# Kernel optimization log

Hardware: AMD Instinct MI355X
Metric: run time of the kernel (lower is better)

Reference implementation:

```python
import jax, jax.numpy as jnp
import numpy as np

B, C, H, W = 8, 96, 56, 56
N = H * W
K = 9
COUT = 2 * C  # 192


def setup_inputs() -> dict:
    key = jax.random.key(0)
    ks = jax.random.split(key, 12)
    s = 0.05
    inp = {
        "x": jax.random.normal(ks[0], (B, C, H, W), jnp.float32),
        "kmap_w": jax.random.normal(ks[1], (C, 500), jnp.float32) * s,
        "kmap_b": jnp.zeros((500,), jnp.float32),
        "kfc_w": jax.random.normal(ks[2], (500, 64), jnp.float32) * s,
        "kfc_b": jnp.zeros((64,), jnp.float32),
        "kmu_w": jax.random.normal(ks[3], (64, 32), jnp.float32) * s,
        "kmu_b": jnp.zeros((32,), jnp.float32),
        "kdec_w": jax.random.normal(ks[4], (32, K), jnp.float32) * s,
        "kdec_b": jnp.zeros((K,), jnp.float32),
        "ec1_w": jax.random.normal(ks[5], (2 * C, C), jnp.float32) * s,
        "ec1_b": jnp.zeros((C,), jnp.float32),
        "ec2_w": jax.random.normal(ks[6], (2 * C, C), jnp.float32) * s,
        "ec2_b": jnp.zeros((C,), jnp.float32),
        "fc_w": jax.random.normal(ks[7], (C, COUT), jnp.float32) * s,
        "fc_b": jnp.zeros((COUT,), jnp.float32),
        "io_w": jax.random.normal(ks[8], (C, COUT), jnp.float32) * s,
        "io_b": jnp.zeros((COUT,), jnp.float32),
        "up_w": jax.random.normal(ks[9], (2 * COUT, COUT), jnp.float32) * s,
        "up_b": jnp.zeros((COUT,), jnp.float32),
    }
    return inp


def reference(x, kmap_w, kmap_b, kfc_w, kfc_b, kmu_w, kmu_b, kdec_w, kdec_b,
              ec1_w, ec1_b, ec2_w, ec2_b, fc_w, fc_b, io_w, io_b, up_w, up_b):
    b, c, h, w = x.shape
    n = h * w
    xf = x.reshape(b, c, n).transpose(0, 2, 1)  # [B, N, C]

    # ---- dense kNN graph (dilation=1, deterministic) ----
    sq = jnp.sum(xf * xf, axis=-1)  # [B, N]
    dist = sq[:, :, None] - 2.0 * jnp.einsum('bnc,bmc->bnm', xf, xf) + sq[:, None, :]
    _, nn_idx = jax.lax.top_k(-dist, K)  # [B, N, K] local neighbor indices

    nodes = xf.reshape(b * n, c)  # flat node features

    # ---- VAE-like K predictor -> per-node kept-degree (non-differentiable) ----
    hK = nodes @ kmap_w + kmap_b
    hK = jax.nn.relu(hK @ kfc_w + kfc_b)
    mu = hK @ kmu_w + kmu_b
    logits = mu @ kdec_w + kdec_b  # [B*N, K]
    k_int = jnp.argmax(logits, axis=1)  # in [0, K-1]

    # edge mask: keep first k_int[i] of node i's K edges
    edge_mask = (jnp.arange(K)[None, :] < k_int[:, None]).reshape(-1)  # [B*N*K]
    emask = edge_mask.astype(nodes.dtype)[:, None]

    # flatten edges with per-batch node offsets (local -> global indices)
    offs = (jnp.arange(b) * n)[:, None, None]
    src = (nn_idx + offs).reshape(-1)              # x_j
    dst = jnp.repeat(jnp.arange(b * n), K)         # x_i (center)

    def edge_conv(feat, wgt, bias):
        xi = feat[dst]
        xj = feat[src]
        msg = jnp.concatenate([xi, xj - xi], axis=-1) @ wgt + bias
        msg = msg * emask  # pruned edges contribute 0 to 'add' aggregation
        return jax.ops.segment_sum(msg, dst, num_segments=b * n)

    h1 = jax.nn.relu(edge_conv(nodes, ec1_w, ec1_b))
    h2 = edge_conv(h1, ec2_w, ec2_b)
    agg = h2 @ fc_w + fc_b                 # EdgeAgg output [B*N, COUT]

    xio = nodes @ io_w + io_b              # inOutFC
    upd = jax.nn.relu(jnp.concatenate([xio, agg], axis=-1) @ up_w + up_b)

    out = upd.reshape(b, n, 2 * c).transpose(0, 2, 1).reshape(b, 2 * c, h, w)
    return out
```

## Files before the change

kernel.cpp:

```cpp
#include <hip/hip_runtime.h>

#define NODES 25088
#define NB 8
#define NPB 3136
#define C 96
#define KNN 9
#define COUT 192
#define MSPLIT 4
#define T12 12
#define NCAND (MSPLIT * T12)

typedef float f32x4 __attribute__((ext_vector_type(4)));
typedef float f32x16 __attribute__((ext_vector_type(16)));
typedef short s16x8 __attribute__((ext_vector_type(8)));

__device__ __forceinline__ unsigned short f2bf(float x) {
  unsigned u = __float_as_uint(x);
  return (unsigned short)((u + 0x7fffu + ((u >> 16) & 1u)) >> 16);
}
__device__ __forceinline__ float bf2f(unsigned short h) {
  return __uint_as_float(((unsigned)h) << 16);
}

__global__ void transpose_kernel(const float* __restrict__ x, float* __restrict__ xf) {
  __shared__ float t[32][33];
  int b = blockIdx.z, ct = blockIdx.y, nt = blockIdx.x;
  int tx = threadIdx.x, ty = threadIdx.y;
  int n0 = nt * 32, c0 = ct * 32;
  const float* xb = x + (size_t)b * C * NPB;
#pragma unroll
  for (int i = 0; i < 4; i++) {
    int c = c0 + ty + i * 8;
    t[ty + i * 8][tx] = xb[(size_t)c * NPB + n0 + tx];
  }
  __syncthreads();
  float* xfb = xf + (size_t)b * NPB * C;
#pragma unroll
  for (int i = 0; i < 4; i++) {
    int n = n0 + ty + i * 8;
    xfb[(size_t)n * C + c0 + tx] = t[tx][ty + i * 8];
  }
}

__global__ void sqsplit_kernel(const float* __restrict__ xf, float* __restrict__ sq,
                               unsigned short* __restrict__ xh,
                               unsigned short* __restrict__ xl) {
  int node = blockIdx.x * 256 + threadIdx.x;
  const float4* r = (const float4*)(xf + (size_t)node * C);
  ushort4* hp = (ushort4*)(xh + (size_t)node * C);
  ushort4* lp = (ushort4*)(xl + (size_t)node * C);
  float s = 0.f;
#pragma unroll
  for (int i = 0; i < 24; i++) {
    float4 v = r[i];
    s += v.x * v.x + v.y * v.y + v.z * v.z + v.w * v.w;
    ushort4 h, l;
    h.x = f2bf(v.x); l.x = f2bf(v.x - bf2f(h.x));
    h.y = f2bf(v.y); l.y = f2bf(v.y - bf2f(h.y));
    h.z = f2bf(v.z); l.z = f2bf(v.z - bf2f(h.z));
    h.w = f2bf(v.w); l.w = f2bf(v.w - bf2f(h.w));
    hp[i] = h;
    lp[i] = l;
  }
  sq[node] = s;
}

__global__ void fold_all_kernel(
    const float* __restrict__ kmap_w, const float* __restrict__ kmap_b,
    const float* __restrict__ kfc_w, const float* __restrict__ kfc_b,
    const float* __restrict__ kmu_w, const float* __restrict__ kmu_b,
    const float* __restrict__ kdec_w, const float* __restrict__ kdec_b,
    const float* __restrict__ ec1_w, const float* __restrict__ ec2_w,
    const float* __restrict__ io_w, const float* __restrict__ io_b,
    const float* __restrict__ fc_w, const float* __restrict__ fc_b,
    const float* __restrict__ up_w, const float* __restrict__ up_b,
    float* __restrict__ WkP, float* __restrict__ bkP, float* __restrict__ WdP,
    float* __restrict__ bdP, float* __restrict__ bPf,
    unsigned short* __restrict__ B1h, unsigned short* __restrict__ B1l,
    unsigned short* __restrict__ B2h, unsigned short* __restrict__ B2l,
    unsigned short* __restrict__ BFh, unsigned short* __restrict__ BFl) {
  __shared__ float sh[4][64];
  int bid = blockIdx.x, tid = threadIdx.x;
  int tx = tid & 63, ty = tid >> 6;
  if (bid < 96) {
    int m = bid;
    float acc = 0.f;
    for (int k = ty; k < 500; k += 4) acc += kmap_w[m * 500 + k] * kfc_w[k * 64 + tx];
    sh[ty][tx] = acc;
    __syncthreads();
    if (ty == 0) WkP[m * 64 + tx] = sh[0][tx] + sh[1][tx] + sh[2][tx] + sh[3][tx];
  } else if (bid == 96) {
    float acc = 0.f;
    for (int k = ty; k < 500; k += 4) acc += kmap_b[k] * kfc_w[k * 64 + tx];
    sh[ty][tx] = acc;
    __syncthreads();
    if (ty == 0) bkP[tx] = sh[0][tx] + sh[1][tx] + sh[2][tx] + sh[3][tx] + kfc_b[tx];
  } else if (bid < 161) {
    int m = bid - 97;
    float acc = 0.f;
    if (tx < 9) {
      for (int k = ty; k < 32; k += 4) acc += kmu_w[m * 32 + k] * kdec_w[k * 9 + tx];
    }
    sh[ty][tx] = acc;
    __syncthreads();
    if (ty == 0 && tx < 9) WdP[m * 9 + tx] = sh[0][tx] + sh[1][tx] + sh[2][tx] + sh[3][tx];
  } else if (bid == 161) {
    float acc = 0.f;
    if (tx < 9) {
      for (int k = ty; k < 32; k += 4) acc += kmu_b[k] * kdec_w[k * 9 + tx];
    }
    sh[ty][tx] = acc;
    __syncthreads();
    if (ty == 0 && tx < 9) bdP[tx] = sh[0][tx] + sh[1][tx] + sh[2][tx] + sh[3][tx] + kdec_b[tx];
  } else if (bid < 234) {
    int t = (bid - 162) * 256 + tid;
    int n = t / 192, k = t % 192;
    float v = ec1_w[(size_t)k * 96 + n];
    if (k < 96) v -= ec1_w[(size_t)(k + 96) * 96 + n];
    unsigned short h = f2bf(v);
    B1h[t] = h;
    B1l[t] = f2bf(v - bf2f(h));
  } else if (bid < 306) {
    int t = (bid - 234) * 256 + tid;
    int n = t / 192, k = t % 192;
    float v = ec2_w[(size_t)k * 96 + n];
    if (k < 96) v -= ec2_w[(size_t)(k + 96) * 96 + n];
    unsigned short h = f2bf(v);
    B2h[t] = h;
    B2l[t] = f2bf(v - bf2f(h));
  } else if (bid < 594) {
    int r = bid - 306;
    int m = r / 3, n = (r % 3) * 64 + tx;
    float acc = 0.f;
    for (int k = ty; k < 192; k += 4) acc += io_w[m * 192 + k] * up_w[(size_t)k * 192 + n];
    sh[ty][tx] = acc;
    __syncthreads();
    if (ty == 0) {
      float v = sh[0][tx] + sh[1][tx] + sh[2][tx] + sh[3][tx];
      unsigned short h = f2bf(v);
      BFh[(size_t)n * 192 + m] = h;
      BFl[(size_t)n * 192 + m] = f2bf(v - bf2f(h));
    }
  } else if (bid < 882) {
    int r = bid - 594;
    int m = r / 3, n = (r % 3) * 64 + tx;
    float acc = 0.f;
    for (int k = ty; k < 192; k += 4)
      acc += fc_w[m * 192 + k] * up_w[(size_t)(192 + k) * 192 + n];
    sh[ty][tx] = acc;
    __syncthreads();
    if (ty == 0) {
      float v = sh[0][tx] + sh[1][tx] + sh[2][tx] + sh[3][tx];
      unsigned short h = f2bf(v);
      BFh[(size_t)n * 192 + 96 + m] = h;
      BFl[(size_t)n * 192 + 96 + m] = f2bf(v - bf2f(h));
    }
  } else {
    if (tid < 192) {
      float acc = up_b[tid];
      for (int k = 0; k < 192; k++) {
        acc += io_b[k] * up_w[k * 192 + tid];
        acc += fc_b[k] * up_w[(192 + k) * 192 + tid];
      }
      bPf[tid] = acc;
    }
  }
}

__global__ __launch_bounds__(256) void gemmhead_kernel(
    const float* __restrict__ A0, const float* __restrict__ B,
    const float* __restrict__ bias, const float* __restrict__ WdP,
    const float* __restrict__ bdP, int* __restrict__ kint,
    float* __restrict__ rs) {
  __shared__ float As[16][68];
  __shared__ float Bs[16][68];
  __shared__ float hs[64][68];
  __shared__ float wd[576];
  __shared__ float bd[9];
  int tid = threadIdx.x;
  int tx = tid & 15, ty = tid >> 4;
  int row0 = blockIdx.x * 64;
  for (int f = tid; f < 576; f += 256) wd[f] = WdP[f];
  if (tid < 9) bd[tid] = bdP[tid];
  float acc[4][4] = {};
  int ai = tid >> 2;
  int ak = (tid & 3) * 4;
  int bk = tid >> 4;
  int bj = (tid & 15) * 4;

  for (int k0 = 0; k0 < 96; k0 += 16) {
    {
      int r = row0 + ai;
      float4 v = *(const float4*)(A0 + (size_t)r * 96 + k0 + ak);
      As[ak + 0][ai] = v.x;
      As[ak + 1][ai] = v.y;
      As[ak + 2][ai] = v.z;
      As[ak + 3][ai] = v.w;
    }
    {
      int kg = k0 + bk;
      float4 v = *(const float4*)(B + (size_t)kg * 64 + bj);
      *(float4*)&Bs[bk][bj] = v;
    }
    __syncthreads();
#pragma unroll
    for (int kk = 0; kk < 16; kk++) {
      float4 av = *(const float4*)&As[kk][ty * 4];
      float4 bv = *(const float4*)&Bs[kk][tx * 4];
      acc[0][0] += av.x * bv.x; acc[0][1] += av.x * bv.y; acc[0][2] += av.x * bv.z; acc[0][3] += av.x * bv.w;
      acc[1][0] += av.y * bv.x; acc[1][1] += av.y * bv.y; acc[1][2] += av.y * bv.z; acc[1][3] += av.y * bv.w;
      acc[2][0] += av.z * bv.x; acc[2][1] += av.z * bv.y; acc[2][2] += av.z * bv.z; acc[2][3] += av.z * bv.w;
      acc[3][0] += av.w * bv.x; acc[3][1] += av.w * bv.y; acc[3][2] += av.w * bv.z; acc[3][3] += av.w * bv.w;
    }
    __syncthreads();
  }
#pragma unroll
  for (int ii = 0; ii < 4; ii++) {
#pragma unroll
    for (int jj = 0; jj < 4; jj++) {
      int j = tx * 4 + jj;
      hs[ty * 4 + ii][j] = fmaxf(acc[ii][jj] + bias[j], 0.f);
    }
  }
  __syncthreads();
  if (tid < 64) {
    int node = row0 + tid;
    const float4* hp = (const float4*)hs[tid];
    float4 h[16];
#pragma unroll
    for (int i = 0; i < 16; i++) h[i] = hp[i];
    float best = -3.4e38f;
    int bi = 0;
#pragma unroll
    for (int n = 0; n < 9; n++) {
      float a = bd[n];
#pragma unroll
      for (int k = 0; k < 16; k++) {
        float4 hv = h[k];
        a += hv.x * wd[(4 * k + 0) * 9 + n] + hv.y * wd[(4 * k + 1) * 9 + n] +
             hv.z * wd[(4 * k + 2) * 9 + n] + hv.w * wd[(4 * k + 3) * 9 + n];
      }
      if (a > best) { best = a; bi = n; }
    }
    kint[node] = bi;
    rs[node] = (float)bi;
  }
}

__device__ __forceinline__ void ce(float& a, float& b) {
  float lo = fminf(a, b);
  b = fmaxf(a, b);
  a = lo;
}

__device__ __forceinline__ void sort16(float* s) {
  ce(s[0], s[1]); ce(s[2], s[3]); ce(s[0], s[2]); ce(s[1], s[3]); ce(s[1], s[2]);
  ce(s[4], s[5]); ce(s[6], s[7]); ce(s[4], s[6]); ce(s[5], s[7]); ce(s[5], s[6]);
  ce(s[0], s[4]); ce(s[1], s[5]); ce(s[2], s[6]); ce(s[3], s[7]);
  ce(s[2], s[4]); ce(s[3], s[5]);
  ce(s[1], s[2]); ce(s[3], s[4]); ce(s[5], s[6]);
  ce(s[8], s[9]); ce(s[10], s[11]); ce(s[8], s[10]); ce(s[9], s[11]); ce(s[9], s[10]);
  ce(s[12], s[13]); ce(s[14], s[15]); ce(s[12], s[14]); ce(s[13], s[15]); ce(s[13], s[14]);
  ce(s[8], s[12]); ce(s[9], s[13]); ce(s[10], s[14]); ce(s[11], s[15]);
  ce(s[10], s[12]); ce(s[11], s[13]);
  ce(s[9], s[10]); ce(s[11], s[12]); ce(s[13], s[14]);
  ce(s[0], s[8]); ce(s[1], s[9]); ce(s[2], s[10]); ce(s[3], s[11]);
  ce(s[4], s[12]); ce(s[5], s[13]); ce(s[6], s[14]); ce(s[7], s[15]);
  ce(s[4], s[8]); ce(s[5], s[9]); ce(s[6], s[10]); ce(s[7], s[11]);
  ce(s[2], s[4]); ce(s[3], s[5]); ce(s[6], s[8]); ce(s[7], s[9]);
  ce(s[10], s[12]); ce(s[11], s[13]);
  ce(s[1], s[2]); ce(s[3], s[4]); ce(s[5], s[6]); ce(s[7], s[8]);
  ce(s[9], s[10]); ce(s[11], s[12]); ce(s[13], s[14]);
}

__device__ __forceinline__ void bmerge16(float* fd, const float* s) {
  float L[16];
#pragma unroll
  for (int i = 0; i < 16; i++) L[i] = fminf(fd[i], s[15 - i]);
  ce(L[0], L[8]); ce(L[1], L[9]); ce(L[2], L[10]); ce(L[3], L[11]);
  ce(L[4], L[12]); ce(L[5], L[13]); ce(L[6], L[14]); ce(L[7], L[15]);
  ce(L[0], L[4]); ce(L[1], L[5]); ce(L[2], L[6]); ce(L[3], L[7]);
  ce(L[8], L[12]); ce(L[9], L[13]); ce(L[10], L[14]); ce(L[11], L[15]);
  ce(L[0], L[2]); ce(L[1], L[3]); ce(L[4], L[6]); ce(L[5], L[7]);
  ce(L[8], L[10]); ce(L[9], L[11]); ce(L[12], L[14]); ce(L[13], L[15]);
  ce(L[0], L[1]); ce(L[2], L[3]); ce(L[4], L[5]); ce(L[6], L[7]);
  ce(L[8], L[9]); ce(L[10], L[11]); ce(L[12], L[13]); ce(L[14], L[15]);
#pragma unroll
  for (int i = 0; i < 16; i++) fd[i] = L[i];
}

__global__ __launch_bounds__(256) void knn_mfma_kernel(
    const unsigned short* __restrict__ xh, const unsigned short* __restrict__ xl,
    const float* __restrict__ sq, int* __restrict__ pk_i) {
  __shared__ __align__(16) float smem_f[256 * 17];
  unsigned short* mh = (unsigned short*)smem_f;
  float* sqs = smem_f + 3328;
  int tid = threadIdx.x;
  int lane = tid & 63, wv = tid >> 6;
  int wm = wv >> 1, wq = wv & 1;
  int b = blockIdx.y, z = blockIdx.z;
  int q0 = blockIdx.x * 64;
  int bbase = b * NPB;
  int t0 = (z * 49) / MSPLIT, t1 = ((z + 1) * 49) / MSPLIT;

  int koff = (lane >> 5) * 8;
  int qrow = bbase + q0 + wq * 32 + (lane & 31);
  s16x8 bqh[6], bql[6];
  {
    const unsigned short* ph = xh + (size_t)qrow * 96 + koff;
    const unsigned short* pl = xl + (size_t)qrow * 96 + koff;
#pragma unroll
    for (int kc = 0; kc < 6; kc++) {
      bqh[kc] = *(const s16x8*)(ph + kc * 16);
      bql[kc] = *(const s16x8*)(pl + kc * 16);
    }
  }
  float sqr = sq[qrow];

  float fd[16];
#pragma unroll
  for (int k = 0; k < 16; k++) fd[k] = 3.4e38f;

  int srow = tid >> 2, sseg = tid & 3;
  int soff = srow * 104 + sseg * 24;

  s16x8 st0, st1, st2;
  float stq = 0.f;
  {
    const unsigned short* gh =
        xh + (size_t)(bbase + t0 * 64 + srow) * 96 + sseg * 24;
    st0 = *(const s16x8*)(gh);
    st1 = *(const s16x8*)(gh + 8);
    st2 = *(const s16x8*)(gh + 16);
    if (tid < 64) stq = sq[bbase + t0 * 64 + tid];
  }

  for (int t = t0; t < t1; t++) {
    __syncthreads();
    *(s16x8*)(mh + soff) = st0;
    *(s16x8*)(mh + soff + 8) = st1;
    *(s16x8*)(mh + soff + 16) = st2;
    if (tid < 64) sqs[tid] = stq;
    __syncthreads();

    int tn = (t + 1 < t1) ? (t + 1) : t;
    {
      const unsigned short* gh =
          xh + (size_t)(bbase + tn * 64 + srow) * 96 + sseg * 24;
      st0 = *(const s16x8*)(gh);
      st1 = *(const s16x8*)(gh + 8);
      st2 = *(const s16x8*)(gh + 16);
      if (tid < 64) stq = sq[bbase + tn * 64 + tid];
    }

    int mrow = wm * 32 + (lane & 31);
    f32x16 acc = (f32x16){0.f, 0.f, 0.f, 0.f, 0.f, 0.f, 0.f, 0.f,
                          0.f, 0.f, 0.f, 0.f, 0.f, 0.f, 0.f, 0.f};
#pragma unroll
    for (int kc = 0; kc < 6; kc++) {
      s16x8 amh = *(const s16x8*)(mh + mrow * 104 + kc * 16 + koff);
      acc = __builtin_amdgcn_mfma_f32_32x32x16_bf16(amh, bqh[kc], acc, 0, 0, 0);
      acc = __builtin_amdgcn_mfma_f32_32x32x16_bf16(amh, bql[kc], acc, 0, 0, 0);
    }

    int lbase = (t - t0) * 64;
    float cs[16];
#pragma unroll
    for (int reg = 0; reg < 16; reg++) {
      int mloc = wm * 32 + (reg & 3) + 8 * (reg >> 2) + 4 * (lane >> 5);
      float d = fmaf(-2.f, acc[reg], sqr + sqs[mloc]);
      unsigned u = (__float_as_uint(d) & 0xFFFFFC00u) | (unsigned)(lbase + mloc);
      cs[reg] = __uint_as_float(u);
    }
    sort16(cs);
    bmerge16(fd, cs);
  }

  __syncthreads();
  float* cd = smem_f;
#pragma unroll
  for (int k = 0; k < 16; k++) cd[(wv * 64 + lane) * 17 + k] = fd[k];
  __syncthreads();
  if (wv == 0) {
    int wva = lane >> 5, ql = lane & 31;
    int ra = wva * 64 + ql, rb = wva * 64 + ql + 32;
    int rc = (wva + 2) * 64 + ql, rd = (wva + 2) * 64 + ql + 32;
    float A[16], B[16];
#pragma unroll
    for (int k = 0; k < 16; k++) { A[k] = cd[ra * 17 + k]; B[k] = cd[rb * 17 + k]; }
    bmerge16(A, B);
    float Cc[16], Dd[16];
#pragma unroll
    for (int k = 0; k < 16; k++) { Cc[k] = cd[rc * 17 + k]; Dd[k] = cd[rd * 17 + k]; }
    bmerge16(Cc, Dd);
    bmerge16(A, Cc);
    size_t base = ((size_t)(bbase + q0 + lane) * MSPLIT + z) * T12;
#pragma unroll
    for (int k = 0; k < T12; k++) {
      int mloc = (int)(__float_as_uint(A[k]) & 0x3FFu) + t0 * 64;
      pk_i[base + k] = bbase + mloc;
    }
  }
}

__global__ __launch_bounds__(256) void rescore_kernel(
    const float* __restrict__ xf, const float* __restrict__ sq,
    const int* __restrict__ pk_i, int* __restrict__ nn) {
  __shared__ float qr[4][96];
  __shared__ float sqq[4];
  int tid = threadIdx.x;
  int qloc = tid >> 6, c = tid & 63;
  int qbase = blockIdx.x * 4;
  for (int f = tid; f < 4 * 96; f += 256)
    qr[f / 96][f % 96] = xf[(size_t)(qbase + f / 96) * 96 + f % 96];
  if (tid < 4) sqq[tid] = sq[qbase + tid];
  __syncthreads();

  int q = qbase + qloc;
  int jv = 0;
  if (c < NCAND) jv = pk_i[(size_t)q * NCAND + c];

  int grp = c >> 3;
  int chunk = c & 7;
  const float4* qp = (const float4*)qr[qloc];
  float4 qv0 = qp[chunk];
  float4 qv1 = qp[chunk + 8];
  float4 qv2 = qp[chunk + 16];

  float dots[6];
#pragma unroll
  for (int it = 0; it < 6; it++) {
    int j = __shfl(jv, it * 8 + grp, 64);
    const float4* mp = (const float4*)(xf + (size_t)j * 96);
    float4 m0 = mp[chunk];
    float4 m1 = mp[chunk + 8];
    float4 m2 = mp[chunk + 16];
    float p = qv0.x * m0.x + qv0.y * m0.y + qv0.z * m0.z + qv0.w * m0.w +
              qv1.x * m1.x + qv1.y * m1.y + qv1.z * m1.z + qv1.w * m1.w +
              qv2.x * m2.x + qv2.y * m2.y + qv2.z * m2.z + qv2.w * m2.w;
    p += __shfl_xor(p, 1, 64);
    p += __shfl_xor(p, 2, 64);
    p += __shfl_xor(p, 4, 64);
    dots[it] = p;
  }

  float g0 = __shfl(dots[0], (c & 7) * 8, 64);
  float g1 = __shfl(dots[1], (c & 7) * 8, 64);
  float g2 = __shfl(dots[2], (c & 7) * 8, 64);
  float g3 = __shfl(dots[3], (c & 7) * 8, 64);
  float g4 = __shfl(dots[4], (c & 7) * 8, 64);
  float g5 = __shfl(dots[5], (c & 7) * 8, 64);
  int itstar = c >> 3;
  float dot = g0;
  dot = (itstar == 1) ? g1 : dot;
  dot = (itstar == 2) ? g2 : dot;
  dot = (itstar == 3) ? g3 : dot;
  dot = (itstar == 4) ? g4 : dot;
  dot = (itstar == 5) ? g5 : dot;

  unsigned long long key = 0xFFFFFFFFFFFFFFFFull;
  if (c < NCAND) {
    float d = (sqq[qloc] - 2.0f * dot) + sq[jv];
    unsigned u = __float_as_uint(d);
    u ^= (u & 0x80000000u) ? 0xFFFFFFFFu : 0x80000000u;
    key = ((unsigned long long)u << 32) | (unsigned)jv;
  }

#pragma unroll
  for (int k = 2; k <= 64; k <<= 1) {
#pragma unroll
    for (int jm = k >> 1; jm >= 1; jm >>= 1) {
      unsigned long long other = __shfl_xor(key, jm, 64);
      bool takeMin = ((c & jm) == 0) == ((c & k) == 0);
      bool sw = (other < key) == takeMin;
      key = sw ? other : key;
    }
  }

  if (c < KNN) {
    nn[(size_t)q * KNN + c] = (int)(unsigned)(key & 0xFFFFFFFFull);
  }
}

__global__ void gather_f32_kernel(const float* __restrict__ feat, const int* __restrict__ nn,
                                  const int* __restrict__ kint,
                                  unsigned short* __restrict__ Sh,
                                  unsigned short* __restrict__ Sl) {
  int idx = blockIdx.x * 256 + threadIdx.x;
  int node = idx / 24, c4 = idx % 24;
  int kc = kint[node];
  const int* nr = nn + (size_t)node * KNN;
  float4 acc = make_float4(0.f, 0.f, 0.f, 0.f);
  for (int k = 0; k < kc; k++) {
    int j = nr[k];
    float4 v = ((const float4*)(feat + (size_t)j * C))[c4];
    acc.x += v.x; acc.y += v.y; acc.z += v.z; acc.w += v.w;
  }
  ushort4 h, l;
  h.x = f2bf(acc.x); l.x = f2bf(acc.x - bf2f(h.x));
  h.y = f2bf(acc.y); l.y = f2bf(acc.y - bf2f(h.y));
  h.z = f2bf(acc.z); l.z = f2bf(acc.z - bf2f(h.z));
  h.w = f2bf(acc.w); l.w = f2bf(acc.w - bf2f(h.w));
  ((ushort4*)(Sh + (size_t)node * C))[c4] = h;
  ((ushort4*)(Sl + (size_t)node * C))[c4] = l;
}

__global__ void gather_bf_kernel(const unsigned short* __restrict__ fh,
                                 const unsigned short* __restrict__ fl,
                                 const int* __restrict__ nn, const int* __restrict__ kint,
                                 unsigned short* __restrict__ Sh,
                                 unsigned short* __restrict__ Sl) {
  int idx = blockIdx.x * 256 + threadIdx.x;
  int node = idx / 24, c4 = idx % 24;
  int kc = kint[node];
  const int* nr = nn + (size_t)node * KNN;
  float4 acc = make_float4(0.f, 0.f, 0.f, 0.f);
  for (int k = 0; k < kc; k++) {
    int j = nr[k];
    ushort4 h = ((const ushort4*)(fh + (size_t)j * C))[c4];
    ushort4 l = ((const ushort4*)(fl + (size_t)j * C))[c4];
    acc.x += bf2f(h.x) + bf2f(l.x);
    acc.y += bf2f(h.y) + bf2f(l.y);
    acc.z += bf2f(h.z) + bf2f(l.z);
    acc.w += bf2f(h.w) + bf2f(l.w);
  }
  ushort4 h, l;
  h.x = f2bf(acc.x); l.x = f2bf(acc.x - bf2f(h.x));
  h.y = f2bf(acc.y); l.y = f2bf(acc.y - bf2f(h.y));
  h.z = f2bf(acc.z); l.z = f2bf(acc.z - bf2f(h.z));
  h.w = f2bf(acc.w); l.w = f2bf(acc.w - bf2f(h.w));
  ((ushort4*)(Sh + (size_t)node * C))[c4] = h;
  ((ushort4*)(Sl + (size_t)node * C))[c4] = l;
}

__global__ __launch_bounds__(192) void mfma_ec_kernel(
    const unsigned short* __restrict__ A0h, const unsigned short* __restrict__ A0l,
    const unsigned short* __restrict__ A1h, const unsigned short* __restrict__ A1l,
    const unsigned short* __restrict__ Bth, const unsigned short* __restrict__ Btl,
    const float* __restrict__ rs, const float* __restrict__ bias, int relu,
    unsigned short* __restrict__ Oh, unsigned short* __restrict__ Ol) {
  __shared__ float rsL[32];
  __shared__ float bL[96];
  int tid = threadIdx.x, lane = tid & 63, wv = tid >> 6;
  int m0 = blockIdx.x * 32;
  if (tid < 32) rsL[tid] = rs[m0 + tid];
  if (tid < 96) bL[tid] = bias[tid];
  __syncthreads();

  int koff = (lane >> 5) * 8;
  int arow = m0 + (lane & 31);
  const unsigned short* a0h = A0h + (size_t)arow * 96 + koff;
  const unsigned short* a0l = A0l + (size_t)arow * 96 + koff;
  const unsigned short* a1h = A1h + (size_t)arow * 96 + koff;
  const unsigned short* a1l = A1l + (size_t)arow * 96 + koff;
  int n = wv * 32 + (lane & 31);

  f32x16 acc1 = (f32x16){0.f, 0.f, 0.f, 0.f, 0.f, 0.f, 0.f, 0.f,
                         0.f, 0.f, 0.f, 0.f, 0.f, 0.f, 0.f, 0.f};
  f32x16 acc2 = acc1;

#pragma unroll
  for (int c = 0; c < 6; c++) {
    s16x8 ah = *(const s16x8*)(a0h + c * 16);
    s16x8 al = *(const s16x8*)(a0l + c * 16);
    size_t bo = (size_t)n * 192 + c * 16 + koff;
    s16x8 bh = *(const s16x8*)(Bth + bo);
    s16x8 bl = *(const s16x8*)(Btl + bo);
    acc1 = __builtin_amdgcn_mfma_f32_32x32x16_bf16(ah, bh, acc1, 0, 0, 0);
    acc1 = __builtin_amdgcn_mfma_f32_32x32x16_bf16(al, bh, acc1, 0, 0, 0);
    acc1 = __builtin_amdgcn_mfma_f32_32x32x16_bf16(ah, bl, acc1, 0, 0, 0);
  }
#pragma unroll
  for (int c = 6; c < 12; c++) {
    s16x8 ah = *(const s16x8*)(a1h + (c - 6) * 16);
    s16x8 al = *(const s16x8*)(a1l + (c - 6) * 16);
    size_t bo = (size_t)n * 192 + c * 16 + koff;
    s16x8 bh = *(const s16x8*)(Bth + bo);
    s16x8 bl = *(const s16x8*)(Btl + bo);
    acc2 = __builtin_amdgcn_mfma_f32_32x32x16_bf16(ah, bh, acc2, 0, 0, 0);
    acc2 = __builtin_amdgcn_mfma_f32_32x32x16_bf16(al, bh, acc2, 0, 0, 0);
    acc2 = __builtin_amdgcn_mfma_f32_32x32x16_bf16(ah, bl, acc2, 0, 0, 0);
  }

  float bn = bL[n];
#pragma unroll
  for (int reg = 0; reg < 16; reg++) {
    int rl = (reg & 3) + 8 * (reg >> 2) + 4 * (lane >> 5);
    int r = m0 + rl;
    float v = rsL[rl] * (acc1[reg] + bn) + acc2[reg];
    if (relu) v = fmaxf(v, 0.f);
    unsigned short h = f2bf(v);
    Oh[(size_t)r * 96 + n] = h;
    Ol[(size_t)r * 96 + n] = f2bf(v - bf2f(h));
  }
}

__global__ __launch_bounds__(192) void mfma_final_kernel(
    const unsigned short* __restrict__ A0h, const unsigned short* __restrict__ A0l,
    const unsigned short* __restrict__ A1h, const unsigned short* __restrict__ A1l,
    const unsigned short* __restrict__ Bth, const unsigned short* __restrict__ Btl,
    const float* __restrict__ bias, float* __restrict__ out) {
  __shared__ float bL[96];
  __shared__ float tt[3][32][33];
  int tid = threadIdx.x, lane = tid & 63, wv = tid >> 6;
  int m0 = blockIdx.x * 32;
  int n0 = blockIdx.y * 96;
  if (tid < 96) bL[tid] = bias[n0 + tid];
  __syncthreads();

  int koff = (lane >> 5) * 8;
  int arow = m0 + (lane & 31);
  const unsigned short* a0h = A0h + (size_t)arow * 96 + koff;
  const unsigned short* a0l = A0l + (size_t)arow * 96 + koff;
  const unsigned short* a1h = A1h + (size_t)arow * 96 + koff;
  const unsigned short* a1l = A1l + (size_t)arow * 96 + koff;
  int nloc = lane & 31;
  int n = n0 + wv * 32 + nloc;

  f32x16 acc = (f32x16){0.f, 0.f, 0.f, 0.f, 0.f, 0.f, 0.f, 0.f,
                        0.f, 0.f, 0.f, 0.f, 0.f, 0.f, 0.f, 0.f};
#pragma unroll
  for (int c = 0; c < 12; c++) {
    s16x8 ah, al;
    if (c < 6) {
      ah = *(const s16x8*)(a0h + c * 16);
      al = *(const s16x8*)(a0l + c * 16);
    } else {
      ah = *(const s16x8*)(a1h + (c - 6) * 16);
      al = *(const s16x8*)(a1l + (c - 6) * 16);
    }
    size_t bo = (size_t)n * 192 + c * 16 + koff;
    s16x8 bh = *(const s16x8*)(Bth + bo);
    s16x8 bl = *(const s16x8*)(Btl + bo);
    acc = __builtin_amdgcn_mfma_f32_32x32x16_bf16(ah, bh, acc, 0, 0, 0);
    acc = __builtin_amdgcn_mfma_f32_32x32x16_bf16(al, bh, acc, 0, 0, 0);
    acc = __builtin_amdgcn_mfma_f32_32x32x16_bf16(ah, bl, acc, 0, 0, 0);
  }

  float bn = bL[wv * 32 + nloc];
#pragma unroll
  for (int reg = 0; reg < 16; reg++) {
    int rl = (reg & 3) + 8 * (reg >> 2) + 4 * (lane >> 5);
    tt[wv][nloc][rl] = fmaxf(acc[reg] + bn, 0.f);
  }
  __builtin_amdgcn_s_waitcnt(0);
  int gbase = m0 + nloc;
  int bb = gbase / NPB, nidx = gbase % NPB;
#pragma unroll
  for (int i = 0; i < 16; i++) {
    int nl = 2 * i + (lane >> 5);
    float v = tt[wv][nl][nloc];
    int ng = n0 + wv * 32 + nl;
    out[(size_t)bb * COUT * NPB + (size_t)ng * NPB + nidx] = v;
  }
}

extern "C" void kernel_launch(void* const* d_in, const int* in_sizes, int n_in,
                              void* d_out, int out_size, void* d_ws, size_t ws_size,
                              hipStream_t stream) {
  const float* x      = (const float*)d_in[0];
  const float* kmap_w = (const float*)d_in[1];
  const float* kmap_b = (const float*)d_in[2];
  const float* kfc_w  = (const float*)d_in[3];
  const float* kfc_b  = (const float*)d_in[4];
  const float* kmu_w  = (const float*)d_in[5];
  const float* kmu_b  = (const float*)d_in[6];
  const float* kdec_w = (const float*)d_in[7];
  const float* kdec_b = (const float*)d_in[8];
  const float* ec1_w  = (const float*)d_in[9];
  const float* ec1_b  = (const float*)d_in[10];
  const float* ec2_w  = (const float*)d_in[11];
  const float* ec2_b  = (const float*)d_in[12];
  const float* fc_w   = (const float*)d_in[13];
  const float* fc_b   = (const float*)d_in[14];
  const float* io_w   = (const float*)d_in[15];
  const float* io_b   = (const float*)d_in[16];
  const float* up_w   = (const float*)d_in[17];
  const float* up_b   = (const float*)d_in[18];

  char* ws = (char*)d_ws;
  size_t off = 0;
  auto alloc = [&](size_t bytes) -> void* {
    void* p = ws + off;
    off += (bytes + 255) & ~(size_t)255;
    return p;
  };
  const size_t HBF = (size_t)NODES * C * 2;
  float* xf   = (float*)alloc((size_t)NODES * C * 4);
  float* sqb  = (float*)alloc((size_t)NODES * 4);
  float* rs   = (float*)alloc((size_t)NODES * 4);
  int*   kint = (int*)alloc((size_t)NODES * 4);
  int*   nn   = (int*)alloc((size_t)NODES * KNN * 4);
  unsigned short* xh = (unsigned short*)alloc(HBF);
  unsigned short* xl = (unsigned short*)alloc(HBF);
  unsigned short* Sh = (unsigned short*)alloc(HBF);
  unsigned short* Sl = (unsigned short*)alloc(HBF);
  char* region = (char*)alloc((size_t)NODES * COUT * 4);
  int*   pk_i   = (int*)region;
  unsigned short* h1h = (unsigned short*)region;
  unsigned short* h1l = (unsigned short*)(region + HBF);
  unsigned short* h2h = (unsigned short*)(region + 2 * HBF);
  unsigned short* h2l = (unsigned short*)(region + 3 * HBF);
  float* WkP = (float*)alloc(96 * 64 * 4);
  float* bkP = (float*)alloc(64 * 4);
  float* WdP = (float*)alloc(64 * 9 * 4);
  float* bdP = (float*)alloc(16 * 4);
  float* bPf = (float*)alloc(192 * 4);
  unsigned short* B1h = (unsigned short*)alloc(96 * 192 * 2);
  unsigned short* B1l = (unsigned short*)alloc(96 * 192 * 2);
  unsigned short* B2h = (unsigned short*)alloc(96 * 192 * 2);
  unsigned short* B2l = (unsigned short*)alloc(96 * 192 * 2);
  unsigned short* BFh = (unsigned short*)alloc(192 * 192 * 2);
  unsigned short* BFl = (unsigned short*)alloc(192 * 192 * 2);

  transpose_kernel<<<dim3(98, 3, 8), dim3(32, 8), 0, stream>>>(x, xf);
  sqsplit_kernel<<<98, 256, 0, stream>>>(xf, sqb, xh, xl);

  fold_all_kernel<<<883, 256, 0, stream>>>(
      kmap_w, kmap_b, kfc_w, kfc_b, kmu_w, kmu_b, kdec_w, kdec_b, ec1_w, ec2_w,
      io_w, io_b, fc_w, fc_b, up_w, up_b,
      WkP, bkP, WdP, bdP, bPf, B1h, B1l, B2h, B2l, BFh, BFl);

  gemmhead_kernel<<<392, 256, 0, stream>>>(xf, WkP, bkP, WdP, bdP, kint, rs);

  knn_mfma_kernel<<<dim3(49, 8, MSPLIT), 256, 0, stream>>>(xh, xl, sqb, pk_i);
  rescore_kernel<<<6272, 256, 0, stream>>>(xf, sqb, pk_i, nn);

  gather_f32_kernel<<<2352, 256, 0, stream>>>(xf, nn, kint, Sh, Sl);
  mfma_ec_kernel<<<784, 192, 0, stream>>>(xh, xl, Sh, Sl, B1h, B1l, rs, ec1_b, 1,
                                          h1h, h1l);
  gather_bf_kernel<<<2352, 256, 0, stream>>>(h1h, h1l, nn, kint, Sh, Sl);
  mfma_ec_kernel<<<784, 192, 0, stream>>>(h1h, h1l, Sh, Sl, B2h, B2l, rs, ec2_b, 0,
                                          h2h, h2l);
  mfma_final_kernel<<<dim3(784, 2), 192, 0, stream>>>(xh, xl, h2h, h2l, BFh, BFl,
                                                      bPf, (float*)d_out);
}
```

Before: 343.1 us.

## Fuse neighbor gather into edge-conv MFMA kernels and shrink kNN merge to 12

The neighbor-sum gather kernels are folded into the edge-conv MFMA kernel, which now sums neighbor features into shared-memory tiles, so the Sh/Sl intermediates and two launches go away. The kNN per-thread candidate list drops from 16 to 12 entries, with a smaller bitonic merge that needs fewer registers and compare-exchanges. Squared norms are read as float4 vectors from shared memory. The fused kernel adds LDS use and puts the irregular gather latency in front of the MFMA work in each block.

Result: no change. 338.3 us (-1.4%).

```diff
diff --git a/kernel.cpp b/kernel.cpp
--- a/kernel.cpp
+++ b/kernel.cpp
@@ -273,20 +273,18 @@
   ce(s[9], s[10]); ce(s[11], s[12]); ce(s[13], s[14]);
 }
 
-__device__ __forceinline__ void bmerge16(float* fd, const float* s) {
-  float L[16];
-#pragma unroll
-  for (int i = 0; i < 16; i++) L[i] = fminf(fd[i], s[15 - i]);
+__device__ __forceinline__ void bmerge12(float* fd, const float* s) {
+  float L[12];
+#pragma unroll
+  for (int i = 0; i < 12; i++) L[i] = fminf(fd[i], s[11 - i]);
   ce(L[0], L[8]); ce(L[1], L[9]); ce(L[2], L[10]); ce(L[3], L[11]);
-  ce(L[4], L[12]); ce(L[5], L[13]); ce(L[6], L[14]); ce(L[7], L[15]);
-  ce(L[0], L[4]); ce(L[1], L[5]); ce(L[2], L[6]); ce(L[3], L[7]);
-  ce(L[8], L[12]); ce(L[9], L[13]); ce(L[10], L[14]); ce(L[11], L[15]);
+  ce(L[4], L[8]); ce(L[5], L[9]); ce(L[6], L[10]); ce(L[7], L[11]);
   ce(L[0], L[2]); ce(L[1], L[3]); ce(L[4], L[6]); ce(L[5], L[7]);
-  ce(L[8], L[10]); ce(L[9], L[11]); ce(L[12], L[14]); ce(L[13], L[15]);
+  ce(L[8], L[10]); ce(L[9], L[11]);
   ce(L[0], L[1]); ce(L[2], L[3]); ce(L[4], L[5]); ce(L[6], L[7]);
-  ce(L[8], L[9]); ce(L[10], L[11]); ce(L[12], L[13]); ce(L[14], L[15]);
-#pragma unroll
-  for (int i = 0; i < 16; i++) fd[i] = L[i];
+  ce(L[8], L[9]); ce(L[10], L[11]);
+#pragma unroll
+  for (int i = 0; i < 12; i++) fd[i] = L[i];
 }
 
 __global__ __launch_bounds__(256) void knn_mfma_kernel(
@@ -317,9 +315,9 @@
   }
   float sqr = sq[qrow];
 
-  float fd[16];
-#pragma unroll
-  for (int k = 0; k < 16; k++) fd[k] = 3.4e38f;
+  float fd[12];
+#pragma unroll
+  for (int k = 0; k < 12; k++) fd[k] = 3.4e38f;
 
   int srow = tid >> 2, sseg = tid & 3;
   int soff = srow * 104 + sseg * 24;
@@ -335,6 +333,8 @@
     if (tid < 64) stq = sq[bbase + t0 * 64 + tid];
   }
 
+  int sqbase = wm * 32 + 4 * (lane >> 5);
+
   for (int t = t0; t < t1; t++) {
     __syncthreads();
     *(s16x8*)(mh + soff) = st0;
@@ -363,37 +363,44 @@
       acc = __builtin_amdgcn_mfma_f32_32x32x16_bf16(amh, bql[kc], acc, 0, 0, 0);
     }
 
+    f32x4 sm0 = *(const f32x4*)(sqs + sqbase);
+    f32x4 sm1 = *(const f32x4*)(sqs + sqbase + 8);
+    f32x4 sm2 = *(const f32x4*)(sqs + sqbase + 16);
+    f32x4 sm3 = *(const f32x4*)(sqs + sqbase + 24);
+
     int lbase = (t - t0) * 64;
     float cs[16];
 #pragma unroll
     for (int reg = 0; reg < 16; reg++) {
-      int mloc = wm * 32 + (reg & 3) + 8 * (reg >> 2) + 4 * (lane >> 5);
-      float d = fmaf(-2.f, acc[reg], sqr + sqs[mloc]);
+      int g = reg >> 2, e = reg & 3;
+      float sqm = (g == 0) ? sm0[e] : (g == 1) ? sm1[e] : (g == 2) ? sm2[e] : sm3[e];
+      int mloc = wm * 32 + e + 8 * g + 4 * (lane >> 5);
+      float d = fmaf(-2.f, acc[reg], sqr + sqm);
       unsigned u = (__float_as_uint(d) & 0xFFFFFC00u) | (unsigned)(lbase + mloc);
       cs[reg] = __uint_as_float(u);
     }
     sort16(cs);
-    bmerge16(fd, cs);
+    bmerge12(fd, cs);
   }
 
   __syncthreads();
   float* cd = smem_f;
 #pragma unroll
-  for (int k = 0; k < 16; k++) cd[(wv * 64 + lane) * 17 + k] = fd[k];
+  for (int k = 0; k < 12; k++) cd[(wv * 64 + lane) * 13 + k] = fd[k];
   __syncthreads();
   if (wv == 0) {
     int wva = lane >> 5, ql = lane & 31;
     int ra = wva * 64 + ql, rb = wva * 64 + ql + 32;
     int rc = (wva + 2) * 64 + ql, rd = (wva + 2) * 64 + ql + 32;
-    float A[16], B[16];
-#pragma unroll
-    for (int k = 0; k < 16; k++) { A[k] = cd[ra * 17 + k]; B[k] = cd[rb * 17 + k]; }
-    bmerge16(A, B);
-    float Cc[16], Dd[16];
-#pragma unroll
-    for (int k = 0; k < 16; k++) { Cc[k] = cd[rc * 17 + k]; Dd[k] = cd[rd * 17 + k]; }
-    bmerge16(Cc, Dd);
-    bmerge16(A, Cc);
+    float A[12], B[12];
+#pragma unroll
+    for (int k = 0; k < 12; k++) { A[k] = cd[ra * 13 + k]; B[k] = cd[rb * 13 + k]; }
+    bmerge12(A, B);
+    float Cc[12], Dd[12];
+#pragma unroll
+    for (int k = 0; k < 12; k++) { Cc[k] = cd[rc * 13 + k]; Dd[k] = cd[rd * 13 + k]; }
+    bmerge12(Cc, Dd);
+    bmerge12(A, Cc);
     size_t base = ((size_t)(bbase + q0 + lane) * MSPLIT + z) * T12;
 #pragma unroll
     for (int k = 0; k < T12; k++) {
@@ -482,77 +489,61 @@
   }
 }
 
-__global__ void gather_f32_kernel(const float* __restrict__ feat, const int* __restrict__ nn,
-                                  const int* __restrict__ kint,
-                                  unsigned short* __restrict__ Sh,
-                                  unsigned short* __restrict__ Sl) {
-  int idx = blockIdx.x * 256 + threadIdx.x;
-  int node = idx / 24, c4 = idx % 24;
-  int kc = kint[node];
-  const int* nr = nn + (size_t)node * KNN;
-  float4 acc = make_float4(0.f, 0.f, 0.f, 0.f);
-  for (int k = 0; k < kc; k++) {
-    int j = nr[k];
-    float4 v = ((const float4*)(feat + (size_t)j * C))[c4];
-    acc.x += v.x; acc.y += v.y; acc.z += v.z; acc.w += v.w;
-  }
-  ushort4 h, l;
-  h.x = f2bf(acc.x); l.x = f2bf(acc.x - bf2f(h.x));
-  h.y = f2bf(acc.y); l.y = f2bf(acc.y - bf2f(h.y));
-  h.z = f2bf(acc.z); l.z = f2bf(acc.z - bf2f(h.z));
-  h.w = f2bf(acc.w); l.w = f2bf(acc.w - bf2f(h.w));
-  ((ushort4*)(Sh + (size_t)node * C))[c4] = h;
-  ((ushort4*)(Sl + (size_t)node * C))[c4] = l;
-}
-
-__global__ void gather_bf_kernel(const unsigned short* __restrict__ fh,
-                                 const unsigned short* __restrict__ fl,
-                                 const int* __restrict__ nn, const int* __restrict__ kint,
-                                 unsigned short* __restrict__ Sh,
-                                 unsigned short* __restrict__ Sl) {
-  int idx = blockIdx.x * 256 + threadIdx.x;
-  int node = idx / 24, c4 = idx % 24;
-  int kc = kint[node];
-  const int* nr = nn + (size_t)node * KNN;
-  float4 acc = make_float4(0.f, 0.f, 0.f, 0.f);
-  for (int k = 0; k < kc; k++) {
-    int j = nr[k];
-    ushort4 h = ((const ushort4*)(fh + (size_t)j * C))[c4];
-    ushort4 l = ((const ushort4*)(fl + (size_t)j * C))[c4];
-    acc.x += bf2f(h.x) + bf2f(l.x);
-    acc.y += bf2f(h.y) + bf2f(l.y);
-    acc.z += bf2f(h.z) + bf2f(l.z);
-    acc.w += bf2f(h.w) + bf2f(l.w);
-  }
-  ushort4 h, l;
-  h.x = f2bf(acc.x); l.x = f2bf(acc.x - bf2f(h.x));
-  h.y = f2bf(acc.y); l.y = f2bf(acc.y - bf2f(h.y));
-  h.z = f2bf(acc.z); l.z = f2bf(acc.z - bf2f(h.z));
-  h.w = f2bf(acc.w); l.w = f2bf(acc.w - bf2f(h.w));
-  ((ushort4*)(Sh + (size_t)node * C))[c4] = h;
-  ((ushort4*)(Sl + (size_t)node * C))[c4] = l;
-}
-
-__global__ __launch_bounds__(192) void mfma_ec_kernel(
+__global__ __launch_bounds__(192) void mfma_ec_fused_kernel(
     const unsigned short* __restrict__ A0h, const unsigned short* __restrict__ A0l,
-    const unsigned short* __restrict__ A1h, const unsigned short* __restrict__ A1l,
+    const float* __restrict__ feat32, const unsigned short* __restrict__ gfh,
+    const unsigned short* __restrict__ gfl, int mode,
+    const int* __restrict__ nn, const int* __restrict__ kint,
     const unsigned short* __restrict__ Bth, const unsigned short* __restrict__ Btl,
     const float* __restrict__ rs, const float* __restrict__ bias, int relu,
     unsigned short* __restrict__ Oh, unsigned short* __restrict__ Ol) {
   __shared__ float rsL[32];
   __shared__ float bL[96];
+  __shared__ __align__(16) unsigned short Sth[32][104];
+  __shared__ __align__(16) unsigned short Stl[32][104];
   int tid = threadIdx.x, lane = tid & 63, wv = tid >> 6;
   int m0 = blockIdx.x * 32;
   if (tid < 32) rsL[tid] = rs[m0 + tid];
   if (tid < 96) bL[tid] = bias[tid];
+
+  for (int it = tid; it < 768; it += 192) {
+    int nl = it / 24, c4 = it % 24;
+    int node = m0 + nl;
+    int kc = kint[node];
+    const int* nr = nn + (size_t)node * KNN;
+    float4 acc = make_float4(0.f, 0.f, 0.f, 0.f);
+    if (mode == 0) {
+      for (int k = 0; k < kc; k++) {
+        int j = nr[k];
+        float4 v = ((const float4*)(feat32 + (size_t)j * C))[c4];
+        acc.x += v.x; acc.y += v.y; acc.z += v.z; acc.w += v.w;
+      }
+    } else {
+      for (int k = 0; k < kc; k++) {
+        int j = nr[k];
+        ushort4 h = ((const ushort4*)(gfh + (size_t)j * C))[c4];
+        ushort4 l = ((const ushort4*)(gfl + (size_t)j * C))[c4];
+        acc.x += bf2f(h.x) + bf2f(l.x);
+        acc.y += bf2f(h.y) + bf2f(l.y);
+        acc.z += bf2f(h.z) + bf2f(l.z);
+        acc.w += bf2f(h.w) + bf2f(l.w);
+      }
+    }
+    ushort4 h, l;
+    h.x = f2bf(acc.x); l.x = f2bf(acc.x - bf2f(h.x));
+    h.y = f2bf(acc.y); l.y = f2bf(acc.y - bf2f(h.y));
+    h.z = f2bf(acc.z); l.z = f2bf(acc.z - bf2f(h.z));
+    h.w = f2bf(acc.w); l.w = f2bf(acc.w - bf2f(h.w));
+    *(ushort4*)&Sth[nl][c4 * 4] = h;
+    *(ushort4*)&Stl[nl][c4 * 4] = l;
+  }
   __syncthreads();
 
   int koff = (lane >> 5) * 8;
   int arow = m0 + (lane & 31);
   const unsigned short* a0h = A0h + (size_t)arow * 96 + koff;
   const unsigned short* a0l = A0l + (size_t)arow * 96 + koff;
-  const unsigned short* a1h = A1h + (size_t)arow * 96 + koff;
-  const unsigned short* a1l = A1l + (size_t)arow * 96 + koff;
+  int rloc = lane & 31;
   int n = wv * 32 + (lane & 31);
 
   f32x16 acc1 = (f32x16){0.f, 0.f, 0.f, 0.f, 0.f, 0.f, 0.f, 0.f,
@@ -572,8 +563,8 @@
   }
 #pragma unroll
   for (int c = 6; c < 12; c++) {
-    s16x8 ah = *(const s16x8*)(a1h + (c - 6) * 16);
-    s16x8 al = *(const s16x8*)(a1l + (c - 6) * 16);
+    s16x8 ah = *(const s16x8*)(&Sth[rloc][(c - 6) * 16 + koff]);
+    s16x8 al = *(const s16x8*)(&Stl[rloc][(c - 6) * 16 + koff]);
     size_t bo = (size_t)n * 192 + c * 16 + koff;
     s16x8 bh = *(const s16x8*)(Bth + bo);
     s16x8 bl = *(const s16x8*)(Btl + bo);
@@ -693,8 +684,6 @@
   int*   nn   = (int*)alloc((size_t)NODES * KNN * 4);
   unsigned short* xh = (unsigned short*)alloc(HBF);
   unsigned short* xl = (unsigned short*)alloc(HBF);
-  unsigned short* Sh = (unsigned short*)alloc(HBF);
-  unsigned short* Sl = (unsigned short*)alloc(HBF);
   char* region = (char*)alloc((size_t)NODES * COUT * 4);
   int*   pk_i   = (int*)region;
   unsigned short* h1h = (unsigned short*)region;
@@ -726,12 +715,12 @@
   knn_mfma_kernel<<<dim3(49, 8, MSPLIT), 256, 0, stream>>>(xh, xl, sqb, pk_i);
   rescore_kernel<<<6272, 256, 0, stream>>>(xf, sqb, pk_i, nn);
 
-  gather_f32_kernel<<<2352, 256, 0, stream>>>(xf, nn, kint, Sh, Sl);
-  mfma_ec_kernel<<<784, 192, 0, stream>>>(xh, xl, Sh, Sl, B1h, B1l, rs, ec1_b, 1,
-                                          h1h, h1l);
-  gather_bf_kernel<<<2352, 256, 0, stream>>>(h1h, h1l, nn, kint, Sh, Sl);
-  mfma_ec_kernel<<<784, 192, 0, stream>>>(h1h, h1l, Sh, Sl, B2h, B2l, rs, ec2_b, 0,
-                                          h2h, h2l);
+  mfma_ec_fused_kernel<<<784, 192, 0, stream>>>(
+      xh, xl, xf, (const unsigned short*)nullptr, (const unsigned short*)nullptr,
+      0, nn, kint, B1h, B1l, rs, ec1_b, 1, h1h, h1l);
+  mfma_ec_fused_kernel<<<784, 192, 0, stream>>>(
+      h1h, h1l, (const float*)nullptr, h1h, h1l,
+      1, nn, kint, B2h, B2l, rs, ec2_b, 0, h2h, h2l);
   mfma_final_kernel<<<dim3(784, 2), 192, 0, stream>>>(xh, xl, h2h, h2l, BFh, BFl,
                                                       bPf, (float*)d_out);
 }
```
